# Optimization experiments

Measured on AMD Instinct MI355X. Metric: run time of the kernel, lower is better.

## Reference

```python
import jax, jax.numpy as jnp
import numpy as np

N_NODES = 100000
N_EDGES = 8192
DEG = 32                      # nodes per hyperedge
NNZ = N_EDGES * DEG
D_IN = 128
D_HID = 128
D_EDGE = 64
EPS = 1e-5


def _batchnorm(x, g, b):
    # normalize per-feature over the batch (dim 0), as a BatchNorm1d in train mode
    mu = jnp.mean(x, axis=0)
    var = jnp.var(x, axis=0)
    return (x - mu) * jax.lax.rsqrt(var + EPS) * g + b


def _hconv(x, src, eid, w, W, b):
    # hypergraph conv: linear -> node->edge weighted sum -> edge->node weighted sum
    h = x @ W + b                                          # [N, Dout]
    m = jax.ops.segment_sum(w[:, None] * h[src], eid, num_segments=N_EDGES)
    out = jax.ops.segment_sum(w[:, None] * m[eid], src, num_segments=N_NODES)
    return out


def setup_inputs() -> dict:
    key = jax.random.key(0)
    ks = jax.random.split(key, 20)
    src = jax.random.randint(ks[0], (NNZ,), 0, N_NODES)
    eid = jnp.arange(NNZ) // DEG                          # every edge id appears DEG times
    edge_index = jnp.stack([src, eid]).astype(jnp.int64)
    s = lambda k, sh, f: jax.random.normal(k, sh, jnp.float32) * f
    return {
        "x": s(ks[1], (N_NODES, D_IN), 1.0),
        "edge_index": edge_index,
        "edge_weight": jax.random.uniform(ks[2], (NNZ,), jnp.float32),
        "edge_features": s(ks[3], (N_EDGES, D_EDGE), 1.0),
        "adj": jax.random.uniform(ks[4], (N_EDGES, N_EDGES), jnp.float32) / N_EDGES,
        "T": 2,
        "norm1_g": jnp.ones((D_IN,), jnp.float32),
        "norm1_b": jnp.zeros((D_IN,), jnp.float32),
        "norm2_g": jnp.ones((D_EDGE,), jnp.float32),
        "norm2_b": jnp.zeros((D_EDGE,), jnp.float32),
        "W1": s(ks[5], (D_IN, D_HID), 0.05),
        "b1": jnp.zeros((D_HID,), jnp.float32),
        "W2": s(ks[6], (D_HID, D_HID), 0.05),
        "b2": jnp.zeros((D_HID,), jnp.float32),
        "Wn": s(ks[7], (D_HID, D_HID), 0.05),
        "We": s(ks[8], (D_EDGE, D_HID), 0.05),
        "Wg": s(ks[9], (D_HID, D_HID), 0.05),
        "cls_w1": s(ks[10], (D_HID, 16), 0.1),
        "cls_b1": jnp.zeros((16,), jnp.float32),
        "cls_w2": s(ks[11], (16, 2), 0.1),
        "cls_b2": jnp.zeros((2,), jnp.float32),
    }


def reference(x, edge_index, edge_weight, edge_features, adj, T,
              norm1_g, norm1_b, norm2_g, norm2_b,
              W1, b1, W2, b2, Wn, We, Wg,
              cls_w1, cls_b1, cls_w2, cls_b2):
    src, eid = edge_index[0], edge_index[1]
    x = _batchnorm(x, norm1_g, norm1_b)
    x = _hconv(x, src, eid, edge_weight, W1, b1)
    x = _hconv(x, src, eid, edge_weight, W2, b2)
    x = jax.nn.relu(x)
    # aggregate_node_features (mean over nodes incident to each hyperedge) —
    # the per-edge Python loop becomes one fused segment reduce
    s = jax.ops.segment_sum(x[src], eid, num_segments=N_EDGES)           # [E, D]
    cnt = jax.ops.segment_sum(jnp.ones_like(eid, jnp.float32), eid, num_segments=N_EDGES)
    node_features = s / jnp.maximum(cnt, 1.0)[:, None]
    ef = _batchnorm(edge_features, norm2_g, norm2_b)
    # edge-level graph convolution with T propagation steps over edge-edge adj
    h = jax.nn.relu(node_features @ Wn + ef @ We)
    for _ in range(T):
        h = jax.nn.relu(adj @ (h @ Wg))
    # classifier head
    out = jax.nn.relu(h @ cls_w1 + cls_b1) @ cls_w2 + cls_b2             # [E, 2]
    return out
```

## Files before the change

kernel.cpp:

```cpp
#include <hip/hip_runtime.h>

#define N_NODESC 100000
#define N_EDGESC 8192
#define DEGC 32
#define DF 128
#define DEF 64
#define EPSV 1e-5f
#define KSPLIT 8
#define KSLICE (N_EDGESC / KSPLIT)

typedef __attribute__((ext_vector_type(8))) short short8;
typedef __attribute__((ext_vector_type(4))) float f32x4;
typedef __attribute__((ext_vector_type(8))) unsigned short ushort8;

typedef const void __attribute__((address_space(1)))* gptr_t;
typedef void __attribute__((address_space(3)))* lptr_t;

__device__ __forceinline__ unsigned short f2bf(float x) {
    union { float f; unsigned u; } v; v.f = x;
    unsigned r = v.u + 0x7fffu + ((v.u >> 16) & 1u);
    return (unsigned short)(r >> 16);
}

template<int DCOL, int RP>
__global__ __launch_bounds__(256) void colstats(const float* __restrict__ X, long nrows,
                                                float* __restrict__ stats) {
    const int f = threadIdx.x % DCOL;
    const int rg = threadIdx.x / DCOL;
    float s = 0.f, s2 = 0.f;
    for (long r = (long)blockIdx.x * RP + rg; r < nrows; r += (long)gridDim.x * RP) {
        float v = X[r * DCOL + f];
        s += v; s2 += v * v;
    }
    __shared__ float l1[256], l2[256];
    l1[threadIdx.x] = s; l2[threadIdx.x] = s2;
    __syncthreads();
    if (threadIdx.x < DCOL) {
        for (int g = 1; g < RP; ++g) { s += l1[threadIdx.x + g * DCOL]; s2 += l2[threadIdx.x + g * DCOL]; }
        atomicAdd(&stats[f], s);
        atomicAdd(&stats[DCOL + f], s2);
    }
}

__global__ void finalize_bn(const float* __restrict__ stats, const float* __restrict__ g,
                            const float* __restrict__ b, float cnt, int dcol,
                            float* __restrict__ ss) {
    int f = threadIdx.x;
    float mean = stats[f] / cnt;
    float var = stats[dcol + f] / cnt - mean * mean;
    float sc = g[f] * rsqrtf(var + EPSV);
    ss[f] = sc;
    ss[dcol + f] = b[f] - mean * sc;
}

__global__ __launch_bounds__(256) void cvt_bf16_k(const float* __restrict__ in,
                                                  unsigned short* __restrict__ o) {
    size_t i = (size_t)blockIdx.x * 256 + threadIdx.x;
    const f32x4* p = (const f32x4*)in + i * 2;
    f32x4 a = p[0], b = p[1];
    ushort8 r;
    r[0] = f2bf(a[0]); r[1] = f2bf(a[1]); r[2] = f2bf(a[2]); r[3] = f2bf(a[3]);
    r[4] = f2bf(b[0]); r[5] = f2bf(b[1]); r[6] = f2bf(b[2]); r[7] = f2bf(b[3]);
    *((ushort8*)o + i) = r;
}

__global__ __launch_bounds__(256) void csr_fill(const int* __restrict__ src,
                                                const float* __restrict__ ew,
                                                int* __restrict__ cnt,
                                                int* __restrict__ se,
                                                float* __restrict__ swt) {
    int i = blockIdx.x * 256 + threadIdx.x;
    int n = src[i];
    int pos = atomicAdd(&cnt[n], 1);
    if (pos < DEGC) {
        se[(size_t)n * DEGC + pos] = i >> 5;
        swt[(size_t)n * DEGC + pos] = ew[i];
    }
}

__global__ __launch_bounds__(256) void node_apply(const float* __restrict__ m,
                                                  const int* __restrict__ cnt,
                                                  const int* __restrict__ se,
                                                  const float* __restrict__ swt,
                                                  float* __restrict__ out) {
    const int n = blockIdx.x * 2 + (threadIdx.x >> 7);
    const int f = threadIdx.x & 127;
    if (n >= N_NODESC) return;
    int d = cnt[n];
    if (d <= 0) return;
    d = min(d, DEGC);
    const size_t base = (size_t)n * DEGC;
    float acc = 0.f;
    for (int p = 0; p < d; ++p) {
        int e = se[base + p];
        float w = swt[base + p];
        acc += w * m[(size_t)e * DF + f];
    }
    out[(size_t)n * DF + f] = acc;
}

template<bool WEIGHTED, bool AFFINE, bool RELU, bool WRITE_SW>
__global__ __launch_bounds__(128) void gather_k(const float* __restrict__ X,
                                                const float* __restrict__ w,
                                                const int* __restrict__ src,
                                                const float* __restrict__ scale,
                                                const float* __restrict__ shift,
                                                float* __restrict__ out,
                                                float* __restrict__ swout,
                                                float mul) {
    const int e = blockIdx.x, f = threadIdx.x;
    const int base = e * DEGC;
    float acc = 0.f, sw = 0.f;
    #pragma unroll
    for (int j = 0; j < DEGC; ++j) {
        int n = src[base + j];
        float wj = WEIGHTED ? w[base + j] : 1.f;
        float v = X[(size_t)n * DF + f];
        if (RELU) v = fmaxf(v, 0.f);
        acc += wj * v;
        sw += wj;
    }
    float r = acc;
    if (AFFINE) r = acc * scale[f] + sw * shift[f];
    out[(size_t)e * DF + f] = r * mul;
    if (WRITE_SW && f == 0) swout[e] = sw;
}

template<int K1, int K2, int NSLICE, bool RELU_IN, bool RELU_OUT, bool BIAS>
__global__ __launch_bounds__(256) void egemm(const float* __restrict__ A1, const float* __restrict__ W1p,
                                             const float* __restrict__ A2, const float* __restrict__ W2p,
                                             const float* __restrict__ sc2, const float* __restrict__ sh2,
                                             const float* __restrict__ bias, const float* __restrict__ swv,
                                             float* __restrict__ C) {
    constexpr int P1 = K1 + 4;
    constexpr int K2c = (K2 > 0) ? K2 : 1;
    constexpr int P2 = K2c + 4;
    constexpr size_t SLSTR = (size_t)N_EDGESC * K1;
    __shared__ float wt1[DF * P1];
    __shared__ float a1c[32 * K1];
    __shared__ float wt2[(K2 > 0) ? DF * P2 : 1];
    __shared__ float a2c[(K2 > 0) ? 32 * K2c : 1];

    const int tid = threadIdx.x;
    const int r0 = blockIdx.x * 32;

    for (int idx = tid; idx < K1 * DF; idx += 256) {
        int k = idx >> 7, c = idx & 127;
        wt1[c * P1 + k] = W1p[idx];
    }
    for (int idx = tid; idx < 32 * K1; idx += 256) {
        float v;
        if constexpr (NSLICE > 1) {
            v = 0.f;
            #pragma unroll
            for (int s = 0; s < NSLICE; ++s) v += A1[s * SLSTR + (size_t)r0 * K1 + idx];
        } else {
            v = A1[(size_t)r0 * K1 + idx];
        }
        if (RELU_IN) v = fmaxf(v, 0.f);
        a1c[idx] = v;
    }
    if constexpr (K2 > 0) {
        for (int idx = tid; idx < K2 * DF; idx += 256) {
            int k = idx >> 7, c = idx & 127;
            wt2[c * P2 + k] = W2p[idx];
        }
        for (int idx = tid; idx < 32 * K2; idx += 256) {
            int k = idx % K2;
            a2c[idx] = A2[(size_t)r0 * K2 + idx] * sc2[k] + sh2[k];
        }
    }
    __syncthreads();

    const int cg = tid & 31, rg = tid >> 5;
    float acc[4][4];
    if constexpr (BIAS) {
        float bl[4], sl[4];
        #pragma unroll
        for (int j = 0; j < 4; ++j) bl[j] = bias[cg * 4 + j];
        #pragma unroll
        for (int i = 0; i < 4; ++i) sl[i] = swv[r0 + rg * 4 + i];
        #pragma unroll
        for (int i = 0; i < 4; ++i)
            #pragma unroll
            for (int j = 0; j < 4; ++j) acc[i][j] = sl[i] * bl[j];
    } else {
        #pragma unroll
        for (int i = 0; i < 4; ++i)
            #pragma unroll
            for (int j = 0; j < 4; ++j) acc[i][j] = 0.f;
    }

    #pragma unroll 4
    for (int k4 = 0; k4 < K1; k4 += 4) {
        f32x4 av[4], wv[4];
        #pragma unroll
        for (int i = 0; i < 4; ++i) av[i] = *(const f32x4*)&a1c[(rg * 4 + i) * K1 + k4];
        #pragma unroll
        for (int j = 0; j < 4; ++j) wv[j] = *(const f32x4*)&wt1[(cg * 4 + j) * P1 + k4];
        #pragma unroll
        for (int i = 0; i < 4; ++i)
            #pragma unroll
            for (int j = 0; j < 4; ++j)
                #pragma unroll
                for (int q = 0; q < 4; ++q) acc[i][j] += av[i][q] * wv[j][q];
    }
    if constexpr (K2 > 0) {
        #pragma unroll 4
        for (int k4 = 0; k4 < K2; k4 += 4) {
            f32x4 av[4], wv[4];
            #pragma unroll
            for (int i = 0; i < 4; ++i) av[i] = *(const f32x4*)&a2c[(rg * 4 + i) * K2 + k4];
            #pragma unroll
            for (int j = 0; j < 4; ++j) wv[j] = *(const f32x4*)&wt2[(cg * 4 + j) * P2 + k4];
            #pragma unroll
            for (int i = 0; i < 4; ++i)
                #pragma unroll
                for (int j = 0; j < 4; ++j)
                    #pragma unroll
                    for (int q = 0; q < 4; ++q) acc[i][j] += av[i][q] * wv[j][q];
        }
    }

    #pragma unroll
    for (int i = 0; i < 4; ++i) {
        f32x4 o;
        #pragma unroll
        for (int j = 0; j < 4; ++j) {
            float v = acc[i][j];
            if (RELU_OUT) v = fmaxf(v, 0.f);
            o[j] = v;
        }
        *(f32x4*)&C[(size_t)(r0 + rg * 4 + i) * DF + cg * 4] = o;
    }
}

__global__ __launch_bounds__(256) void transp_cvt(const float* __restrict__ Y,
                                                  unsigned short* __restrict__ Yt) {
    __shared__ float t[32][33];
    const int r0 = blockIdx.x * 32, c0 = blockIdx.y * 32;
    const int tc = threadIdx.x & 31, tr = threadIdx.x >> 5;
    #pragma unroll
    for (int i = 0; i < 4; ++i)
        t[tr + i * 8][tc] = Y[(size_t)(r0 + tr + i * 8) * DF + c0 + tc];
    __syncthreads();
    #pragma unroll
    for (int i = 0; i < 4; ++i) {
        int c = tr + i * 8;
        Yt[(size_t)(c0 + c) * N_EDGESC + r0 + tc] = f2bf(t[tc][c]);
    }
}

__global__ __launch_bounds__(256, 2) void adj_gemm(const unsigned short* __restrict__ A,
                                                   const unsigned short* __restrict__ Bt,
                                                   float* __restrict__ H) {
    __shared__ unsigned short sA[2][128 * 64];
    __shared__ unsigned short sB[2][128 * 64];
    const int tid = threadIdx.x;
    const int lane = tid & 63, wave = tid >> 6;
    const int mb = blockIdx.x & 63, ks = blockIdx.x >> 6;
    const size_t m0 = (size_t)mb * 128;
    const int k0 = ks * KSLICE;
    const int wm = wave >> 1, wn = wave & 1;
    float* __restrict__ Hs = H + (size_t)ks * (N_EDGESC * DF);

    f32x4 acc[4][4];
    #pragma unroll
    for (int i = 0; i < 4; ++i)
        #pragma unroll
        for (int j = 0; j < 4; ++j) acc[i][j] = 0.f;

    auto stage = [&](int buf, int kc) {
        #pragma unroll
        for (int i = 0; i < 4; ++i) {
            int slot = i * 256 + wave * 64 + lane;
            int row = slot >> 3, ch = slot & 7;
            int sc = (ch ^ (row & 7)) << 3;
            const unsigned short* ga = A + (m0 + row) * (size_t)N_EDGESC + kc + sc;
            const unsigned short* gb = Bt + (size_t)row * N_EDGESC + kc + sc;
            unsigned short* la = &sA[buf][(i * 256 + wave * 64) * 8];
            unsigned short* lb = &sB[buf][(i * 256 + wave * 64) * 8];
            __builtin_amdgcn_global_load_lds((gptr_t)ga, (lptr_t)la, 16, 0, 0);
            __builtin_amdgcn_global_load_lds((gptr_t)gb, (lptr_t)lb, 16, 0, 0);
        }
    };

    stage(0, k0);
    int cur = 0;
    for (int c = 0; c < KSLICE / 64; ++c) {
        __syncthreads();
        if (c + 1 < KSLICE / 64) stage(cur ^ 1, k0 + (c + 1) * 64);
        #pragma unroll
        for (int kk = 0; kk < 2; ++kk) {
            short8 af[4], bv[4];
            const int chb = kk * 4 + (lane >> 4);
            #pragma unroll
            for (int mf = 0; mf < 4; ++mf) {
                int row = wm * 64 + mf * 16 + (lane & 15);
                af[mf] = *(const short8*)&sA[cur][(row * 8 + (chb ^ (row & 7))) * 8];
            }
            #pragma unroll
            for (int nf = 0; nf < 4; ++nf) {
                int row = wn * 64 + nf * 16 + (lane & 15);
                bv[nf] = *(const short8*)&sB[cur][(row * 8 + (chb ^ (row & 7))) * 8];
            }
            #pragma unroll
            for (int mf = 0; mf < 4; ++mf)
                #pragma unroll
                for (int nf = 0; nf < 4; ++nf)
                    acc[mf][nf] = __builtin_amdgcn_mfma_f32_16x16x32_bf16(af[mf], bv[nf], acc[mf][nf], 0, 0, 0);
        }
        cur ^= 1;
    }

    #pragma unroll
    for (int mf = 0; mf < 4; ++mf)
        #pragma unroll
        for (int nf = 0; nf < 4; ++nf)
            #pragma unroll
            for (int r = 0; r < 4; ++r) {
                size_t row = m0 + wm * 64 + mf * 16 + (lane >> 4) * 4 + r;
                int col = wn * 64 + nf * 16 + (lane & 15);
                Hs[row * DF + col] = acc[mf][nf][r];
            }
}

__global__ __launch_bounds__(256) void classifier_k(const float* __restrict__ H,
                                                    const float* __restrict__ w1, const float* __restrict__ b1,
                                                    const float* __restrict__ w2, const float* __restrict__ b2,
                                                    float* __restrict__ out) {
    constexpr size_t SLSTR = (size_t)N_EDGESC * DF;
    __shared__ float hl[16 * DF];
    __shared__ float w1l[DF * 16];
    __shared__ float hid[16 * 16];
    const int tid = threadIdx.x;
    const int e0 = blockIdx.x * 16;
    for (int idx = tid; idx < 16 * DF; idx += 256) {
        float v = 0.f;
        #pragma unroll
        for (int s = 0; s < KSPLIT; ++s) v += H[s * SLSTR + (size_t)e0 * DF + idx];
        hl[idx] = fmaxf(v, 0.f);
    }
    for (int idx = tid; idx < DF * 16; idx += 256) w1l[idx] = w1[idx];
    __syncthreads();
    {
        int el = tid >> 4, j = tid & 15;
        float a = b1[j];
        for (int k = 0; k < DF; ++k) a += hl[el * DF + k] * w1l[k * 16 + j];
        hid[el * 16 + j] = fmaxf(a, 0.f);
    }
    __syncthreads();
    if (tid < 32) {
        int e = tid >> 1, o = tid & 1;
        float s = b2[o];
        for (int jj = 0; jj < 16; ++jj) s += hid[e * 16 + jj] * w2[jj * 2 + o];
        out[(size_t)(e0 + e) * 2 + o] = s;
    }
}

extern "C" void kernel_launch(void* const* d_in, const int* in_sizes, int n_in,
                              void* d_out, int out_size, void* d_ws, size_t ws_size,
                              hipStream_t stream) {
    const float* x   = (const float*)d_in[0];
    const int*  src  = (const int*)d_in[1];
    const float* ew  = (const float*)d_in[2];
    const float* ef  = (const float*)d_in[3];
    const float* adj = (const float*)d_in[4];
    const float* n1g = (const float*)d_in[6];
    const float* n1b = (const float*)d_in[7];
    const float* n2g = (const float*)d_in[8];
    const float* n2b = (const float*)d_in[9];
    const float* W1  = (const float*)d_in[10];
    const float* b1  = (const float*)d_in[11];
    const float* W2  = (const float*)d_in[12];
    const float* b2  = (const float*)d_in[13];
    const float* Wn  = (const float*)d_in[14];
    const float* We  = (const float*)d_in[15];
    const float* Wg  = (const float*)d_in[16];
    const float* cw1 = (const float*)d_in[17];
    const float* cb1 = (const float*)d_in[18];
    const float* cw2 = (const float*)d_in[19];
    const float* cb2 = (const float*)d_in[20];
    float* out = (float*)d_out;

    float* stats  = (float*)d_ws;
    float* ssx    = stats + 256;
    float* statse = stats + 512;
    float* sse    = stats + 640;
    float* sw     = stats + 1024;
    int*   cnt    = (int*)(sw + 8192);
    int*   se     = cnt + N_NODESC;
    float* swt    = (float*)(se + (size_t)N_NODESC * DEGC);
    float* EB0    = swt + (size_t)N_NODESC * DEGC;
    float* EB1    = EB0 + (size_t)N_EDGESC * DF;
    float* HS     = EB1 + (size_t)N_EDGESC * DF;
    float* NODES  = HS + (size_t)KSPLIT * N_EDGESC * DF;
    unsigned short* yT    = (unsigned short*)(NODES + (size_t)N_NODESC * DF);
    unsigned short* adjbf = yT + (size_t)DF * N_EDGESC;

    hipMemsetAsync(stats, 0, (1024 + 8192) * sizeof(float) + N_NODESC * sizeof(int), stream);

    colstats<128, 2><<<400, 256, 0, stream>>>(x, N_NODESC, stats);
    colstats<64, 4><<<64, 256, 0, stream>>>(ef, N_EDGESC, statse);
    finalize_bn<<<1, 128, 0, stream>>>(stats, n1g, n1b, (float)N_NODESC, 128, ssx);
    finalize_bn<<<1, 64, 0, stream>>>(statse, n2g, n2b, (float)N_EDGESC, 64, sse);

    cvt_bf16_k<<<(N_EDGESC * (N_EDGESC / 8)) / 256, 256, 0, stream>>>(adj, adjbf);

    csr_fill<<<(N_EDGESC * DEGC) / 256, 256, 0, stream>>>(src, ew, cnt, se, swt);

    gather_k<true, true, false, true><<<N_EDGESC, 128, 0, stream>>>(x, ew, src, ssx, ssx + 128, EB0, sw, 1.f);
    egemm<128, 0, 1, false, false, true><<<256, 256, 0, stream>>>(EB0, W1, nullptr, nullptr, nullptr, nullptr, b1, sw, EB1);
    node_apply<<<N_NODESC / 2, 256, 0, stream>>>(EB1, cnt, se, swt, NODES);

    gather_k<true, false, false, false><<<N_EDGESC, 128, 0, stream>>>(NODES, ew, src, nullptr, nullptr, EB0, nullptr, 1.f);
    egemm<128, 0, 1, false, false, true><<<256, 256, 0, stream>>>(EB0, W2, nullptr, nullptr, nullptr, nullptr, b2, sw, EB1);
    node_apply<<<N_NODESC / 2, 256, 0, stream>>>(EB1, cnt, se, swt, NODES);

    gather_k<false, false, true, false><<<N_EDGESC, 128, 0, stream>>>(NODES, nullptr, src, nullptr, nullptr, EB0, nullptr, 1.f / DEGC);

    egemm<128, 64, 1, false, true, false><<<256, 256, 0, stream>>>(EB0, Wn, ef, We, sse, sse + 64, nullptr, nullptr, EB1);

    egemm<128, 0, 1, false, false, false><<<256, 256, 0, stream>>>(EB1, Wg, nullptr, nullptr, nullptr, nullptr, nullptr, nullptr, NODES);
    transp_cvt<<<dim3(256, 4), 256, 0, stream>>>(NODES, yT);
    adj_gemm<<<64 * KSPLIT, 256, 0, stream>>>(adjbf, yT, HS);
    egemm<128, 0, KSPLIT, true, false, false><<<256, 256, 0, stream>>>(HS, Wg, nullptr, nullptr, nullptr, nullptr, nullptr, nullptr, NODES);
    transp_cvt<<<dim3(256, 4), 256, 0, stream>>>(NODES, yT);
    adj_gemm<<<64 * KSPLIT, 256, 0, stream>>>(adjbf, yT, HS);

    classifier_k<<<N_EDGESC / 16, 256, 0, stream>>>(HS, cw1, cb1, cw2, cb2, out);
}
```

Measured before the change: 532.2 us.

## Fuse adj bf16 conversion into first adj GEMM and transposed bf16 egemm output

Removes the standalone fp32→bf16 conversion of the 8192x8192 adjacency by converting tiles inside the first adj_gemm pass, which also writes the bf16 copy for reuse in the second pass. The Wg egemm now writes its output directly in transposed bf16 form, so both transp_cvt kernels disappear. The two BN finalize kernels are merged into one launch, and the weight tile in shared memory uses an XOR swizzle instead of padding. The first adj_gemm loses async global-to-LDS loads for A and gains register conversion plus an extra global store, and the transposed output writes are narrow and strided.

Result: slower. 546.9 us (+2.8%).

```diff
diff --git a/kernel.cpp b/kernel.cpp
--- a/kernel.cpp
+++ b/kernel.cpp
@@ -12,6 +12,7 @@
 typedef __attribute__((ext_vector_type(8))) short short8;
 typedef __attribute__((ext_vector_type(4))) float f32x4;
 typedef __attribute__((ext_vector_type(8))) unsigned short ushort8;
+typedef __attribute__((ext_vector_type(4))) unsigned short u16x4;
 
 typedef const void __attribute__((address_space(1)))* gptr_t;
 typedef void __attribute__((address_space(3)))* lptr_t;
@@ -42,26 +43,25 @@
     }
 }
 
-__global__ void finalize_bn(const float* __restrict__ stats, const float* __restrict__ g,
-                            const float* __restrict__ b, float cnt, int dcol,
-                            float* __restrict__ ss) {
-    int f = threadIdx.x;
-    float mean = stats[f] / cnt;
-    float var = stats[dcol + f] / cnt - mean * mean;
-    float sc = g[f] * rsqrtf(var + EPSV);
-    ss[f] = sc;
-    ss[dcol + f] = b[f] - mean * sc;
-}
-
-__global__ __launch_bounds__(256) void cvt_bf16_k(const float* __restrict__ in,
-                                                  unsigned short* __restrict__ o) {
-    size_t i = (size_t)blockIdx.x * 256 + threadIdx.x;
-    const f32x4* p = (const f32x4*)in + i * 2;
-    f32x4 a = p[0], b = p[1];
-    ushort8 r;
-    r[0] = f2bf(a[0]); r[1] = f2bf(a[1]); r[2] = f2bf(a[2]); r[3] = f2bf(a[3]);
-    r[4] = f2bf(b[0]); r[5] = f2bf(b[1]); r[6] = f2bf(b[2]); r[7] = f2bf(b[3]);
-    *((ushort8*)o + i) = r;
+__global__ void finalize_both(const float* __restrict__ stats,
+                              const float* __restrict__ g1, const float* __restrict__ b1,
+                              const float* __restrict__ g2, const float* __restrict__ b2,
+                              float* __restrict__ ssx, float* __restrict__ sse) {
+    int t = threadIdx.x;
+    if (t < 128) {
+        float mean = stats[t] / (float)N_NODESC;
+        float var = stats[128 + t] / (float)N_NODESC - mean * mean;
+        float sc = g1[t] * rsqrtf(var + EPSV);
+        ssx[t] = sc;
+        ssx[128 + t] = b1[t] - mean * sc;
+    } else {
+        int f = t - 128;
+        float mean = stats[512 + f] / (float)N_EDGESC;
+        float var = stats[576 + f] / (float)N_EDGESC - mean * mean;
+        float sc = g2[f] * rsqrtf(var + EPSV);
+        sse[f] = sc;
+        sse[64 + f] = b2[f] - mean * sc;
+    }
 }
 
 __global__ __launch_bounds__(256) void csr_fill(const int* __restrict__ src,
@@ -126,19 +126,17 @@
     if (WRITE_SW && f == 0) swout[e] = sw;
 }
 
-template<int K1, int K2, int NSLICE, bool RELU_IN, bool RELU_OUT, bool BIAS>
+template<int K1, int K2, int NSLICE, bool RELU_IN, bool RELU_OUT, bool BIAS, bool TBF16>
 __global__ __launch_bounds__(256) void egemm(const float* __restrict__ A1, const float* __restrict__ W1p,
                                              const float* __restrict__ A2, const float* __restrict__ W2p,
                                              const float* __restrict__ sc2, const float* __restrict__ sh2,
                                              const float* __restrict__ bias, const float* __restrict__ swv,
-                                             float* __restrict__ C) {
-    constexpr int P1 = K1 + 4;
+                                             float* __restrict__ C, unsigned short* __restrict__ Ct) {
     constexpr int K2c = (K2 > 0) ? K2 : 1;
-    constexpr int P2 = K2c + 4;
     constexpr size_t SLSTR = (size_t)N_EDGESC * K1;
-    __shared__ float wt1[DF * P1];
+    __shared__ float wt1[DF * K1];
     __shared__ float a1c[32 * K1];
-    __shared__ float wt2[(K2 > 0) ? DF * P2 : 1];
+    __shared__ float wt2[(K2 > 0) ? DF * K2c : 1];
     __shared__ float a2c[(K2 > 0) ? 32 * K2c : 1];
 
     const int tid = threadIdx.x;
@@ -146,7 +144,8 @@
 
     for (int idx = tid; idx < K1 * DF; idx += 256) {
         int k = idx >> 7, c = idx & 127;
-        wt1[c * P1 + k] = W1p[idx];
+        int pc = (k >> 2) ^ ((c >> 3) & 7);
+        wt1[c * K1 + pc * 4 + (k & 3)] = W1p[idx];
     }
     for (int idx = tid; idx < 32 * K1; idx += 256) {
         float v;
@@ -163,7 +162,8 @@
     if constexpr (K2 > 0) {
         for (int idx = tid; idx < K2 * DF; idx += 256) {
             int k = idx >> 7, c = idx & 127;
-            wt2[c * P2 + k] = W2p[idx];
+            int pc = (k >> 2) ^ ((c >> 3) & 7);
+            wt2[c * K2c + pc * 4 + (k & 3)] = W2p[idx];
         }
         for (int idx = tid; idx < 32 * K2; idx += 256) {
             int k = idx % K2;
@@ -173,6 +173,7 @@
     __syncthreads();
 
     const int cg = tid & 31, rg = tid >> 5;
+    const int swz = (cg >> 1) & 7;
     float acc[4][4];
     if constexpr (BIAS) {
         float bl[4], sl[4];
@@ -194,10 +195,11 @@
     #pragma unroll 4
     for (int k4 = 0; k4 < K1; k4 += 4) {
         f32x4 av[4], wv[4];
+        const int pk = (((k4 >> 2) ^ swz) << 2);
         #pragma unroll
         for (int i = 0; i < 4; ++i) av[i] = *(const f32x4*)&a1c[(rg * 4 + i) * K1 + k4];
         #pragma unroll
-        for (int j = 0; j < 4; ++j) wv[j] = *(const f32x4*)&wt1[(cg * 4 + j) * P1 + k4];
+        for (int j = 0; j < 4; ++j) wv[j] = *(const f32x4*)&wt1[(cg * 4 + j) * K1 + pk];
         #pragma unroll
         for (int i = 0; i < 4; ++i)
             #pragma unroll
@@ -209,10 +211,11 @@
         #pragma unroll 4
         for (int k4 = 0; k4 < K2; k4 += 4) {
             f32x4 av[4], wv[4];
-            #pragma unroll
-            for (int i = 0; i < 4; ++i) av[i] = *(const f32x4*)&a2c[(rg * 4 + i) * K2 + k4];
-            #pragma unroll
-            for (int j = 0; j < 4; ++j) wv[j] = *(const f32x4*)&wt2[(cg * 4 + j) * P2 + k4];
+            const int pk = (((k4 >> 2) ^ swz) << 2);
+            #pragma unroll
+            for (int i = 0; i < 4; ++i) av[i] = *(const f32x4*)&a2c[(rg * 4 + i) * K2c + k4];
+            #pragma unroll
+            for (int j = 0; j < 4; ++j) wv[j] = *(const f32x4*)&wt2[(cg * 4 + j) * K2c + pk];
             #pragma unroll
             for (int i = 0; i < 4; ++i)
                 #pragma unroll
@@ -222,36 +225,37 @@
         }
     }
 
-    #pragma unroll
-    for (int i = 0; i < 4; ++i) {
-        f32x4 o;
+    if constexpr (TBF16) {
         #pragma unroll
         for (int j = 0; j < 4; ++j) {
-            float v = acc[i][j];
-            if (RELU_OUT) v = fmaxf(v, 0.f);
-            o[j] = v;
-        }
-        *(f32x4*)&C[(size_t)(r0 + rg * 4 + i) * DF + cg * 4] = o;
-    }
-}
-
-__global__ __launch_bounds__(256) void transp_cvt(const float* __restrict__ Y,
-                                                  unsigned short* __restrict__ Yt) {
-    __shared__ float t[32][33];
-    const int r0 = blockIdx.x * 32, c0 = blockIdx.y * 32;
-    const int tc = threadIdx.x & 31, tr = threadIdx.x >> 5;
-    #pragma unroll
-    for (int i = 0; i < 4; ++i)
-        t[tr + i * 8][tc] = Y[(size_t)(r0 + tr + i * 8) * DF + c0 + tc];
-    __syncthreads();
-    #pragma unroll
-    for (int i = 0; i < 4; ++i) {
-        int c = tr + i * 8;
-        Yt[(size_t)(c0 + c) * N_EDGESC + r0 + tc] = f2bf(t[tc][c]);
-    }
-}
-
-__global__ __launch_bounds__(256, 2) void adj_gemm(const unsigned short* __restrict__ A,
+            u16x4 o;
+            #pragma unroll
+            for (int i = 0; i < 4; ++i) {
+                float v = acc[i][j];
+                if (RELU_OUT) v = fmaxf(v, 0.f);
+                o[i] = f2bf(v);
+            }
+            *(u16x4*)&Ct[(size_t)(cg * 4 + j) * N_EDGESC + r0 + rg * 4] = o;
+        }
+    } else {
+        #pragma unroll
+        for (int i = 0; i < 4; ++i) {
+            f32x4 o;
+            #pragma unroll
+            for (int j = 0; j < 4; ++j) {
+                float v = acc[i][j];
+                if (RELU_OUT) v = fmaxf(v, 0.f);
+                o[j] = v;
+            }
+            *(f32x4*)&C[(size_t)(r0 + rg * 4 + i) * DF + cg * 4] = o;
+        }
+    }
+}
+
+template<bool CVT>
+__global__ __launch_bounds__(256, 2) void adj_gemm(const unsigned short* __restrict__ Abf,
+                                                   const float* __restrict__ Af32,
+                                                   unsigned short* __restrict__ Aout,
                                                    const unsigned short* __restrict__ Bt,
                                                    float* __restrict__ H) {
     __shared__ unsigned short sA[2][128 * 64];
@@ -276,11 +280,22 @@
             int slot = i * 256 + wave * 64 + lane;
             int row = slot >> 3, ch = slot & 7;
             int sc = (ch ^ (row & 7)) << 3;
-            const unsigned short* ga = A + (m0 + row) * (size_t)N_EDGESC + kc + sc;
+            if constexpr (CVT) {
+                const float* ga = Af32 + (m0 + row) * (size_t)N_EDGESC + kc + sc;
+                f32x4 a = *(const f32x4*)ga;
+                f32x4 b = *(const f32x4*)(ga + 4);
+                ushort8 r;
+                r[0] = f2bf(a[0]); r[1] = f2bf(a[1]); r[2] = f2bf(a[2]); r[3] = f2bf(a[3]);
+                r[4] = f2bf(b[0]); r[5] = f2bf(b[1]); r[6] = f2bf(b[2]); r[7] = f2bf(b[3]);
+                *(ushort8*)&sA[buf][slot * 8] = r;
+                *(ushort8*)(Aout + (m0 + row) * (size_t)N_EDGESC + kc + sc) = r;
+            } else {
+                const unsigned short* ga = Abf + (m0 + row) * (size_t)N_EDGESC + kc + sc;
+                unsigned short* la = &sA[buf][(i * 256 + wave * 64) * 8];
+                __builtin_amdgcn_global_load_lds((gptr_t)ga, (lptr_t)la, 16, 0, 0);
+            }
             const unsigned short* gb = Bt + (size_t)row * N_EDGESC + kc + sc;
-            unsigned short* la = &sA[buf][(i * 256 + wave * 64) * 8];
             unsigned short* lb = &sB[buf][(i * 256 + wave * 64) * 8];
-            __builtin_amdgcn_global_load_lds((gptr_t)ga, (lptr_t)la, 16, 0, 0);
             __builtin_amdgcn_global_load_lds((gptr_t)gb, (lptr_t)lb, 16, 0, 0);
         }
     };
@@ -385,7 +400,6 @@
 
     float* stats  = (float*)d_ws;
     float* ssx    = stats + 256;
-    float* statse = stats + 512;
     float* sse    = stats + 640;
     float* sw     = stats + 1024;
     int*   cnt    = (int*)(sw + 8192);
@@ -398,35 +412,30 @@
     unsigned short* yT    = (unsigned short*)(NODES + (size_t)N_NODESC * DF);
     unsigned short* adjbf = yT + (size_t)DF * N_EDGESC;
 
-    hipMemsetAsync(stats, 0, (1024 + 8192) * sizeof(float) + N_NODESC * sizeof(int), stream);
+    (void)hipMemsetAsync(stats, 0, (1024 + 8192) * sizeof(float) + N_NODESC * sizeof(int), stream);
 
     colstats<128, 2><<<400, 256, 0, stream>>>(x, N_NODESC, stats);
-    colstats<64, 4><<<64, 256, 0, stream>>>(ef, N_EDGESC, statse);
-    finalize_bn<<<1, 128, 0, stream>>>(stats, n1g, n1b, (float)N_NODESC, 128, ssx);
-    finalize_bn<<<1, 64, 0, stream>>>(statse, n2g, n2b, (float)N_EDGESC, 64, sse);
-
-    cvt_bf16_k<<<(N_EDGESC * (N_EDGESC / 8)) / 256, 256, 0, stream>>>(adj, adjbf);
+    colstats<64, 4><<<64, 256, 0, stream>>>(ef, N_EDGESC, stats + 512);
+    finalize_both<<<1, 192, 0, stream>>>(stats, n1g, n1b, n2g, n2b, ssx, sse);
 
     csr_fill<<<(N_EDGESC * DEGC) / 256, 256, 0, stream>>>(src, ew, cnt, se, swt);
 
     gather_k<true, true, false, true><<<N_EDGESC, 128, 0, stream>>>(x, ew, src, ssx, ssx + 128, EB0, sw, 1.f);
-    egemm<128, 0, 1, false, false, true><<<256, 256, 0, stream>>>(EB0, W1, nullptr, nullptr, nullptr, nullptr, b1, sw, EB1);
+    egemm<128, 0, 1, false, false, true, false><<<256, 256, 0, stream>>>(EB0, W1, nullptr, nullptr, nullptr, nullptr, b1, sw, EB1, nullptr);
     node_apply<<<N_NODESC / 2, 256, 0, stream>>>(EB1, cnt, se, swt, NODES);
 
     gather_k<true, false, false, false><<<N_EDGESC, 128, 0, stream>>>(NODES, ew, src, nullptr, nullptr, EB0, nullptr, 1.f);
-    egemm<128, 0, 1, false, false, true><<<256, 256, 0, stream>>>(EB0, W2, nullptr, nullptr, nullptr, nullptr, b2, sw, EB1);
+    egemm<128, 0, 1, false, false, true, false><<<256, 256, 0, stream>>>(EB0, W2, nullptr, nullptr, nullptr, nullptr, b2, sw, EB1, nullptr);
     node_apply<<<N_NODESC / 2, 256, 0, stream>>>(EB1, cnt, se, swt, NODES);
 
     gather_k<false, false, true, false><<<N_EDGESC, 128, 0, stream>>>(NODES, nullptr, src, nullptr, nullptr, EB0, nullptr, 1.f / DEGC);
 
-    egemm<128, 64, 1, false, true, false><<<256, 256, 0, stream>>>(EB0, Wn, ef, We, sse, sse + 64, nullptr, nullptr, EB1);
-
-    egemm<128, 0, 1, false, false, false><<<256, 256, 0, stream>>>(EB1, Wg, nullptr, nullptr, nullptr, nullptr, nullptr, nullptr, NODES);
-    transp_cvt<<<dim3(256, 4), 256, 0, stream>>>(NODES, yT);
-    adj_gemm<<<64 * KSPLIT, 256, 0, stream>>>(adjbf, yT, HS);
-    egemm<128, 0, KSPLIT, true, false, false><<<256, 256, 0, stream>>>(HS, Wg, nullptr, nullptr, nullptr, nullptr, nullptr, nullptr, NODES);
-    transp_cvt<<<dim3(256, 4), 256, 0, stream>>>(NODES, yT);
-    adj_gemm<<<64 * KSPLIT, 256, 0, stream>>>(adjbf, yT, HS);
+    egemm<128, 64, 1, false, true, false, false><<<256, 256, 0, stream>>>(EB0, Wn, ef, We, sse, sse + 64, nullptr, nullptr, EB1, nullptr);
+
+    egemm<128, 0, 1, false, false, false, true><<<256, 256, 0, stream>>>(EB1, Wg, nullptr, nullptr, nullptr, nullptr, nullptr, nullptr, nullptr, yT);
+    adj_gemm<true><<<64 * KSPLIT, 256, 0, stream>>>(nullptr, adj, adjbf, yT, HS);
+    egemm<128, 0, KSPLIT, true, false, false, true><<<256, 256, 0, stream>>>(HS, Wg, nullptr, nullptr, nullptr, nullptr, nullptr, nullptr, nullptr, yT);
+    adj_gemm<false><<<64 * KSPLIT, 256, 0, stream>>>(adjbf, nullptr, nullptr, yT, HS);
 
     classifier_k<<<N_EDGESC / 16, 256, 0, stream>>>(HS, cw1, cb1, cw2, cb2, out);
 }
```
